# Kernel optimization log

Measured on AMD Instinct MI355X. Metric: run time of the kernel, lower is better.

The kernel has to match this reference:

```python
import jax, jax.numpy as jnp
import numpy as np

NUM_LAYERS = 2
FEATURES = 128
INPUT_SIZE = 128
HIDDEN = 512
BATCH = 128
SEQ_LEN = 512
PRED_LEN = 128


def _uniform(key, shape, fan):
    bound = 1.0 / np.sqrt(fan)
    return jax.random.uniform(key, shape, jnp.float32, -bound, bound)


def setup_inputs() -> dict:
    key = jax.random.key(0)
    ks = jax.random.split(key, 14)
    inp = {}
    inp["x"] = jax.random.normal(ks[0], (BATCH, SEQ_LEN, FEATURES), jnp.float32)
    # encoder Linear(features -> input_size)
    inp["enc_w"] = _uniform(ks[1], (INPUT_SIZE, FEATURES), FEATURES)
    inp["enc_b"] = _uniform(ks[2], (INPUT_SIZE,), FEATURES)
    # decoder Linear(hidden -> input_size)
    inp["dec_w"] = _uniform(ks[3], (INPUT_SIZE, HIDDEN), HIDDEN)
    inp["dec_b"] = _uniform(ks[4], (INPUT_SIZE,), HIDDEN)
    # LSTM layer 0 (input_size -> hidden), gate order i,f,g,o as in PyTorch
    inp["wih0"] = _uniform(ks[5], (4 * HIDDEN, INPUT_SIZE), HIDDEN)
    inp["whh0"] = _uniform(ks[6], (4 * HIDDEN, HIDDEN), HIDDEN)
    inp["bih0"] = _uniform(ks[7], (4 * HIDDEN,), HIDDEN)
    inp["bhh0"] = _uniform(ks[8], (4 * HIDDEN,), HIDDEN)
    # LSTM layer 1 (hidden -> hidden)
    inp["wih1"] = _uniform(ks[9], (4 * HIDDEN, HIDDEN), HIDDEN)
    inp["whh1"] = _uniform(ks[10], (4 * HIDDEN, HIDDEN), HIDDEN)
    inp["bih1"] = _uniform(ks[11], (4 * HIDDEN,), HIDDEN)
    inp["bhh1"] = _uniform(ks[12], (4 * HIDDEN,), HIDDEN)
    inp["pred_len"] = PRED_LEN
    return inp


def _lstm_cell(h, c, inp, wih, whh, bih, bhh):
    g = inp @ wih.T + bih + h @ whh.T + bhh  # [B, 4H]
    i, f, gg, o = jnp.split(g, 4, axis=-1)
    c = jax.nn.sigmoid(f) * c + jax.nn.sigmoid(i) * jnp.tanh(gg)
    h = jax.nn.sigmoid(o) * jnp.tanh(c)
    return h, c


def reference(x, enc_w, enc_b, dec_w, dec_b, wih0, whh0, bih0, bhh0,
              wih1, whh1, bih1, bhh1, pred_len):
    B, S, Fdim = x.shape
    T = S + pred_len - 1
    # pad x to T steps; beyond S the input comes from the previous output
    x_pad = jnp.concatenate([x, jnp.zeros((B, pred_len - 1, Fdim), x.dtype)], axis=1)
    x_t = jnp.transpose(x_pad, (1, 0, 2))  # [T, B, F]

    def step(carry, xs):
        h0, c0, h1, c1, prev_out = carry
        xt, t = xs
        inp = jnp.where(t < S, xt, prev_out)
        e = inp @ enc_w.T + enc_b                    # encoder
        h0, c0 = _lstm_cell(h0, c0, e, wih0, whh0, bih0, bhh0)
        h1, c1 = _lstm_cell(h1, c1, h0, wih1, whh1, bih1, bhh1)
        out = h1 @ dec_w.T + dec_b                   # decoder
        return (h0, c0, h1, c1, out), out

    z = jnp.zeros((B, HIDDEN), x.dtype)
    init = (z, z, z, z, jnp.zeros((B, Fdim), x.dtype))
    _, outs = jax.lax.scan(step, init, (x_t, jnp.arange(T)))
    # keep steps idx >= S-1 (pred_len outputs), back to [B, pred_len, input_size]
    return jnp.transpose(outs[S - 1:], (1, 0, 2))
```

## Files before the change

kernel.cpp:

```cpp
#include <hip/hip_runtime.h>
#include <math.h>

#define HID 512
#define FEAT 128
#define SEQL 512
#define PREDL 128
#define NWG 256
#define HK 516
#define EK 132

__device__ __forceinline__ float sigf_(float x) { return 1.0f / (1.0f + __expf(-x)); }
__device__ __forceinline__ float tanh_(float x) {
  float ax = fabsf(x);
  float e2 = __expf(-2.0f * ax);
  return copysignf((1.0f - e2) / (1.0f + e2), x);
}

__device__ __forceinline__ void stg_sc(float* p, float v) {
  __hip_atomic_store(p, v, __ATOMIC_RELAXED, __HIP_MEMORY_SCOPE_AGENT);
}

__device__ __forceinline__ void bar_arrive(int* __restrict__ bar, int grp,
                                           int phase, int tid, bool& last) {
  __syncthreads();
  if (tid == 0) {
    const int a = __hip_atomic_fetch_add(bar + grp * 32, 1, __ATOMIC_RELAXED,
                                         __HIP_MEMORY_SCOPE_AGENT);
    last = (a == 32 * phase - 1);
    if (last)
      __hip_atomic_store(bar + 512 + grp * 32, phase, __ATOMIC_RELAXED,
                         __HIP_MEMORY_SCOPE_AGENT);
  }
  asm volatile("" ::: "memory");
}
__device__ __forceinline__ void bar_wait(int* __restrict__ bar, int grp,
                                         int phase, int tid, bool last) {
  asm volatile("" ::: "memory");
  if (tid == 0 && !last) {
    while (__hip_atomic_load(bar + 512 + grp * 32, __ATOMIC_RELAXED,
                             __HIP_MEMORY_SCOPE_AGENT) < phase)
      __builtin_amdgcn_s_sleep(1);
  }
  __syncthreads();
}

__device__ __forceinline__ void stage_h(float* __restrict__ dst,
                                        const float* __restrict__ src,
                                        int b0, int tid) {
  const int kb = tid >> 2;
  const int bq = (tid & 3) * 4;
  const float* p0 = src + ((size_t)kb) * 128 + b0 + bq;
  const float* p1 = src + ((size_t)kb + 128) * 128 + b0 + bq;
  const float* p2 = src + ((size_t)kb + 256) * 128 + b0 + bq;
  const float* p3 = src + ((size_t)kb + 384) * 128 + b0 + bq;
  float4 r0, r1, r2, r3;
  asm volatile(
      "global_load_dwordx4 %0, %4, off sc0 sc1\n\t"
      "global_load_dwordx4 %1, %5, off sc0 sc1\n\t"
      "global_load_dwordx4 %2, %6, off sc0 sc1\n\t"
      "global_load_dwordx4 %3, %7, off sc0 sc1\n\t"
      "s_waitcnt vmcnt(0)"
      : "=&v"(r0), "=&v"(r1), "=&v"(r2), "=&v"(r3)
      : "v"(p0), "v"(p1), "v"(p2), "v"(p3)
      : "memory");
  dst[(bq + 0) * HK + kb] = r0.x;  dst[(bq + 1) * HK + kb] = r0.y;
  dst[(bq + 2) * HK + kb] = r0.z;  dst[(bq + 3) * HK + kb] = r0.w;
  dst[(bq + 0) * HK + kb + 128] = r1.x;  dst[(bq + 1) * HK + kb + 128] = r1.y;
  dst[(bq + 2) * HK + kb + 128] = r1.z;  dst[(bq + 3) * HK + kb + 128] = r1.w;
  dst[(bq + 0) * HK + kb + 256] = r2.x;  dst[(bq + 1) * HK + kb + 256] = r2.y;
  dst[(bq + 2) * HK + kb + 256] = r2.z;  dst[(bq + 3) * HK + kb + 256] = r2.w;
  dst[(bq + 0) * HK + kb + 384] = r3.x;  dst[(bq + 1) * HK + kb + 384] = r3.y;
  dst[(bq + 2) * HK + kb + 384] = r3.z;  dst[(bq + 3) * HK + kb + 384] = r3.w;
}

__device__ __forceinline__ void stage_x(float* __restrict__ dst,
                                        const float* __restrict__ x, int t,
                                        int b0, int tid) {
  const int bb = tid >> 5;
  const int fq = (tid & 31) * 4;
  const float4 v =
      *(const float4*)(x + ((size_t)(b0 + bb) * SEQL + t) * FEAT + fq);
  *(float4*)(dst + bb * EK + fq) = v;
}

__device__ __forceinline__ void gemv512(float& a0, float& a1, float& a2,
                                        float& a3, const float* __restrict__ s,
                                        const float4* __restrict__ w0,
                                        const float4* __restrict__ w1,
                                        const float4* __restrict__ w2,
                                        const float4* __restrict__ w3) {
#pragma unroll 2
  for (int k4 = 0; k4 < 128; ++k4) {
    const float4 sv = *(const float4*)(s + k4 * 4);
    float4 w;
    w = w0[k4]; a0 += w.x * sv.x + w.y * sv.y + w.z * sv.z + w.w * sv.w;
    w = w1[k4]; a1 += w.x * sv.x + w.y * sv.y + w.z * sv.z + w.w * sv.w;
    w = w2[k4]; a2 += w.x * sv.x + w.y * sv.y + w.z * sv.z + w.w * sv.w;
    w = w3[k4]; a3 += w.x * sv.x + w.y * sv.y + w.z * sv.z + w.w * sv.w;
  }
}
__device__ __forceinline__ void gemv128(float& a0, float& a1, float& a2,
                                        float& a3, const float* __restrict__ s,
                                        const float4* __restrict__ w0,
                                        const float4* __restrict__ w1,
                                        const float4* __restrict__ w2,
                                        const float4* __restrict__ w3) {
#pragma unroll 4
  for (int k4 = 0; k4 < 32; ++k4) {
    const float4 sv = *(const float4*)(s + k4 * 4);
    float4 w;
    w = w0[k4]; a0 += w.x * sv.x + w.y * sv.y + w.z * sv.z + w.w * sv.w;
    w = w1[k4]; a1 += w.x * sv.x + w.y * sv.y + w.z * sv.z + w.w * sv.w;
    w = w2[k4]; a2 += w.x * sv.x + w.y * sv.y + w.z * sv.z + w.w * sv.w;
    w = w3[k4]; a3 += w.x * sv.x + w.y * sv.y + w.z * sv.z + w.w * sv.w;
  }
}

__device__ __forceinline__ void act_store(float a0, float a1, float a2,
                                          float a3, float& c_reg,
                                          float* __restrict__ HoutT,
                                          size_t cit) {
  const float ig = sigf_(a0), fg = sigf_(a1);
  const float gg = tanh_(a2), og = sigf_(a3);
  const float cn = fg * c_reg + ig * gg;
  c_reg = cn;
  stg_sc(HoutT + cit, og * tanh_(cn));
}

__global__ __launch_bounds__(512, 2) void k_persist(
    const float* __restrict__ x,
    const float* __restrict__ enc_w, const float* __restrict__ enc_b,
    const float* __restrict__ wih0, const float* __restrict__ whh0,
    const float* __restrict__ bih0, const float* __restrict__ bhh0,
    const float* __restrict__ wih1, const float* __restrict__ whh1,
    const float* __restrict__ bih1, const float* __restrict__ bhh1,
    const float* __restrict__ dec_w, const float* __restrict__ dec_b,
    const float* __restrict__ Wcomp, const float* __restrict__ bcomp,
    float* __restrict__ h0A, float* __restrict__ h0B,
    float* __restrict__ h1A, float* __restrict__ h1B,
    int* __restrict__ bar, float* __restrict__ out) {
  __shared__ float s_h0[16 * HK];
  __shared__ float s_h1[16 * HK];
  __shared__ float s_x[16 * EK];
  __shared__ float s_e[16 * EK];

  const int wg = blockIdx.x;
  const int tid = threadIdx.x;
  const int ut = (wg & 7) * 4 + ((wg >> 3) & 3);
  const int bt = wg >> 5;
  const int b0 = bt * 16;
  const int half = tid >> 8;
  const int t8 = tid & 255;
  const int u = t8 >> 4, b = t8 & 15;
  const int ug = ut * 16 + u;
  const size_t cit = (size_t)ug * 128 + b0 + b;

  float* h0b[2] = {h0A, h0B};
  float* h1b[2] = {h1A, h1B};
  const float* sh0row = s_h0 + b * HK;
  const float* sh1row = s_h1 + b * HK;
  const float* serow  = s_e + b * EK;

  const float4* e0p = (const float4*)(wih0 + (size_t)ug * FEAT);
  const float4* e1p = (const float4*)(wih0 + (size_t)(512 + ug) * FEAT);
  const float4* e2p = (const float4*)(wih0 + (size_t)(1024 + ug) * FEAT);
  const float4* e3p = (const float4*)(wih0 + (size_t)(1536 + ug) * FEAT);
  const float4* H00 = (const float4*)(whh0 + (size_t)ug * HID);
  const float4* H01 = (const float4*)(whh0 + (size_t)(512 + ug) * HID);
  const float4* H02 = (const float4*)(whh0 + (size_t)(1024 + ug) * HID);
  const float4* H03 = (const float4*)(whh0 + (size_t)(1536 + ug) * HID);
  const float4* Wc0 = (const float4*)(Wcomp + (size_t)ug * HID);
  const float4* Wc1 = (const float4*)(Wcomp + (size_t)(512 + ug) * HID);
  const float4* Wc2 = (const float4*)(Wcomp + (size_t)(1024 + ug) * HID);
  const float4* Wc3 = (const float4*)(Wcomp + (size_t)(1536 + ug) * HID);
  const float4* I10 = (const float4*)(wih1 + (size_t)ug * HID);
  const float4* I11 = (const float4*)(wih1 + (size_t)(512 + ug) * HID);
  const float4* I12 = (const float4*)(wih1 + (size_t)(1024 + ug) * HID);
  const float4* I13 = (const float4*)(wih1 + (size_t)(1536 + ug) * HID);
  const float4* H10 = (const float4*)(whh1 + (size_t)ug * HID);
  const float4* H11 = (const float4*)(whh1 + (size_t)(512 + ug) * HID);
  const float4* H12 = (const float4*)(whh1 + (size_t)(1024 + ug) * HID);
  const float4* H13 = (const float4*)(whh1 + (size_t)(1536 + ug) * HID);
  const float bt00 = bih0[ug] + bhh0[ug];
  const float bt01 = bih0[512 + ug] + bhh0[512 + ug];
  const float bt02 = bih0[1024 + ug] + bhh0[1024 + ug];
  const float bt03 = bih0[1536 + ug] + bhh0[1536 + ug];
  const float ba00 = bt00 + bcomp[ug];
  const float ba01 = bt01 + bcomp[512 + ug];
  const float ba02 = bt02 + bcomp[1024 + ug];
  const float ba03 = bt03 + bcomp[1536 + ug];
  const float b10 = bih1[ug] + bhh1[ug];
  const float b11 = bih1[512 + ug] + bhh1[512 + ug];
  const float b12 = bih1[1024 + ug] + bhh1[1024 + ug];
  const float b13 = bih1[1536 + ug] + bhh1[1536 + ug];

  const int eb = tid & 15;
  const int f0 = (tid >> 4) * 4;
  const float4* ew0 = (const float4*)(enc_w + (size_t)f0 * FEAT);
  const float4* ew1 = (const float4*)(enc_w + (size_t)(f0 + 1) * FEAT);
  const float4* ew2 = (const float4*)(enc_w + (size_t)(f0 + 2) * FEAT);
  const float4* ew3 = (const float4*)(enc_w + (size_t)(f0 + 3) * FEAT);
  const float encb0 = enc_b[f0], encb1 = enc_b[f0 + 1];
  const float encb2 = enc_b[f0 + 2], encb3 = enc_b[f0 + 3];
  const float* sxrow = s_x + eb * EK;

  const int is_dec = (half == 1) && (((wg >> 3) & 3) == 0);
  const int jdec = (wg & 7) * 16 + (t8 >> 4);
  const int bd = t8 & 15;
  const float4* decr = (const float4*)(dec_w + (size_t)jdec * HID);
  const float decb = dec_b[jdec];

  float c_reg = 0.0f;
  int ph = 0;
  bool last = false;

  stage_x(s_x, x, 0, b0, tid);
  for (int t = 0; t < SEQL; ++t) {
    const float* h0in = h0b[(t + 1) & 1];
    float* h0out = h0b[t & 1];
    const float* h1in = h1b[t & 1];
    float* h1out = h1b[(t + 1) & 1];

    stage_h(s_h0, h0in, b0, tid);
    stage_h(s_h1, h1in, b0, tid);
    __syncthreads();

    {
      float a0 = encb0, a1 = encb1, a2 = encb2, a3 = encb3;
      gemv128(a0, a1, a2, a3, sxrow, ew0, ew1, ew2, ew3);
      *(float4*)(s_e + eb * EK + f0) = make_float4(a0, a1, a2, a3);
    }
    __syncthreads();

    if (half == 0) {
      float a0 = bt00, a1 = bt01, a2 = bt02, a3 = bt03;
      gemv512(a0, a1, a2, a3, sh0row, H00, H01, H02, H03);
      gemv128(a0, a1, a2, a3, serow, e0p, e1p, e2p, e3p);
      act_store(a0, a1, a2, a3, c_reg, h0out, cit);
    } else if (t > 0) {
      float a0 = b10, a1 = b11, a2 = b12, a3 = b13;
      gemv512(a0, a1, a2, a3, sh0row, I10, I11, I12, I13);
      gemv512(a0, a1, a2, a3, sh1row, H10, H11, H12, H13);
      act_store(a0, a1, a2, a3, c_reg, h1out, cit);
    }
    bar_arrive(bar, bt, ++ph, tid, last);
    if (t + 1 < SEQL) stage_x(s_x, x, t + 1, b0, tid);
    bar_wait(bar, bt, ph, tid, last);
  }

  stage_h(s_h0, h0b[1], b0, tid);
  stage_h(s_h1, h1b[0], b0, tid);
  __syncthreads();
  if (half == 1) {
    float a0 = b10, a1 = b11, a2 = b12, a3 = b13;
    gemv512(a0, a1, a2, a3, sh0row, I10, I11, I12, I13);
    gemv512(a0, a1, a2, a3, sh1row, H10, H11, H12, H13);
    act_store(a0, a1, a2, a3, c_reg, h1b[1], cit);
  }
  bar_arrive(bar, bt, ++ph, tid, last);
  bar_wait(bar, bt, ph, tid, last);

  for (int t = SEQL; t < SEQL + PREDL - 1; ++t) {
    const float* h1prev = h1b[(t + 1) & 1];
    const float* h0prev = h0b[(t + 1) & 1];
    float* h0cur = h0b[t & 1];
    float* h1cur = h1b[t & 1];

    stage_h(s_h1, h1prev, b0, tid);
    stage_h(s_h0, h0prev, b0, tid);
    __syncthreads();
    if (half == 0) {
      float a0 = ba00, a1 = ba01, a2 = ba02, a3 = ba03;
      gemv512(a0, a1, a2, a3, sh1row, Wc0, Wc1, Wc2, Wc3);
      gemv512(a0, a1, a2, a3, sh0row, H00, H01, H02, H03);
      act_store(a0, a1, a2, a3, c_reg, h0cur, cit);
    } else if (is_dec) {
      float acc = decb;
      const float* srow = s_h1 + bd * HK;
#pragma unroll 2
      for (int k4 = 0; k4 < 128; ++k4) {
        const float4 sv = *(const float4*)(srow + k4 * 4);
        const float4 w = decr[k4];
        acc += w.x * sv.x + w.y * sv.y + w.z * sv.z + w.w * sv.w;
      }
      out[((size_t)(b0 + bd) * PREDL + (t - SEQL)) * FEAT + jdec] = acc;
    }
    bar_arrive(bar, bt, ++ph, tid, last);
    bar_wait(bar, bt, ph, tid, last);

    stage_h(s_h0, h0cur, b0, tid);
    __syncthreads();
    if (half == 1) {
      float a0 = b10, a1 = b11, a2 = b12, a3 = b13;
      gemv512(a0, a1, a2, a3, sh0row, I10, I11, I12, I13);
      gemv512(a0, a1, a2, a3, sh1row, H10, H11, H12, H13);
      act_store(a0, a1, a2, a3, c_reg, h1cur, cit);
    }
    bar_arrive(bar, bt, ++ph, tid, last);
    bar_wait(bar, bt, ph, tid, last);
  }

  stage_h(s_h1, h1b[0], b0, tid);
  __syncthreads();
  if (is_dec) {
    float acc = decb;
    const float* srow = s_h1 + bd * HK;
#pragma unroll 2
    for (int k4 = 0; k4 < 128; ++k4) {
      const float4 sv = *(const float4*)(srow + k4 * 4);
      const float4 w = decr[k4];
      acc += w.x * sv.x + w.y * sv.y + w.z * sv.z + w.w * sv.w;
    }
    out[((size_t)(b0 + bd) * PREDL + (PREDL - 1)) * FEAT + jdec] = acc;
  }
}

__global__ void k_b1(const float* __restrict__ enc_w,
                     const float* __restrict__ dec_w, float* __restrict__ B1) {
  const int idx = blockIdx.x * 256 + threadIdx.x;
  const int j = idx >> 9, m = idx & 511;
  float acc = 0.0f;
  for (int k = 0; k < FEAT; ++k) acc += enc_w[j * FEAT + k] * dec_w[k * HID + m];
  B1[idx] = acc;
}
__global__ void k_wcomp(const float* __restrict__ wih0,
                        const float* __restrict__ B1, float* __restrict__ W) {
  const size_t idx = (size_t)blockIdx.x * 256 + threadIdx.x;
  const int n = (int)(idx >> 9), m = (int)(idx & 511);
  float acc = 0.0f;
  for (int k = 0; k < FEAT; ++k) acc += wih0[n * FEAT + k] * B1[k * HID + m];
  W[idx] = acc;
}
__global__ void k_te(const float* __restrict__ enc_w,
                     const float* __restrict__ enc_b,
                     const float* __restrict__ dec_b, float* __restrict__ te) {
  const int j = threadIdx.x;
  float acc = enc_b[j];
  for (int k = 0; k < FEAT; ++k) acc += dec_b[k] * enc_w[j * FEAT + k];
  te[j] = acc;
}
__global__ void k_bcomp(const float* __restrict__ wih0,
                        const float* __restrict__ te, float* __restrict__ bc) {
  const int n = blockIdx.x * 256 + threadIdx.x;
  float acc = 0.0f;
  for (int j = 0; j < FEAT; ++j) acc += wih0[n * FEAT + j] * te[j];
  bc[n] = acc;
}

extern "C" void kernel_launch(void* const* d_in, const int* in_sizes, int n_in,
                              void* d_out, int out_size, void* d_ws,
                              size_t ws_size, hipStream_t stream) {
  const float* x     = (const float*)d_in[0];
  const float* enc_w = (const float*)d_in[1];
  const float* enc_b = (const float*)d_in[2];
  const float* dec_w = (const float*)d_in[3];
  const float* dec_b = (const float*)d_in[4];
  const float* wih0  = (const float*)d_in[5];
  const float* whh0  = (const float*)d_in[6];
  const float* bih0  = (const float*)d_in[7];
  const float* bhh0  = (const float*)d_in[8];
  const float* wih1  = (const float*)d_in[9];
  const float* whh1  = (const float*)d_in[10];
  const float* bih1  = (const float*)d_in[11];
  const float* bhh1  = (const float*)d_in[12];
  float* out = (float*)d_out;

  float* ws = (float*)d_ws;
  float* h0A   = ws;
  float* h0B   = ws + 65536;
  float* h1A   = ws + 131072;
  float* h1B   = ws + 196608;
  int*   bar   = (int*)(ws + 262144);
  float* Wcomp = ws + 263168;
  float* B1    = ws + 1311744;
  float* te    = ws + 1377280;
  float* bcomp = ws + 1377408;

  hipMemsetAsync(ws, 0, (size_t)263168 * sizeof(float) + 4096, stream);

  k_b1<<<256, 256, 0, stream>>>(enc_w, dec_w, B1);
  k_wcomp<<<4096, 256, 0, stream>>>(wih0, B1, Wcomp);
  k_te<<<1, 128, 0, stream>>>(enc_w, enc_b, dec_b, te);
  k_bcomp<<<8, 256, 0, stream>>>(wih0, te, bcomp);

  k_persist<<<NWG, 512, 0, stream>>>(
      x, enc_w, enc_b, wih0, whh0, bih0, bhh0, wih1, whh1, bih1, bhh1,
      dec_w, dec_b, Wcomp, bcomp, h0A, h0B, h1A, h1B, bar, out);
}
```

Measured before the change: 38.40 ms.

## Interleave gate weights for packed FMA and split-K autoregressive steps across halves

Precomputes gate-interleaved weight layouts (Wa8, Wf8, wih04, enc4) so each thread reads all four gates for one k with a single float4 and accumulates with packed 2-wide FMAs. In the autoregressive phase both thread halves now split the K dimension of each cell and reduce through shared memory, and the decoder is spread across all threads with an 8-way split-K. Both h buffers are staged with one batched load sequence, and launch bounds drop to one block per CU. The goal is to cut the serial per-step GEMV latency and underused threads. The cost is extra prep kernels, more shared memory and syncs, and lower occupancy.

```diff
diff --git a/kernel.cpp b/kernel.cpp
--- a/kernel.cpp
+++ b/kernel.cpp
@@ -8,6 +8,8 @@
 #define NWG 256
 #define HK 516
 #define EK 132
+
+typedef float v2f __attribute__((ext_vector_type(2)));
 
 __device__ __forceinline__ float sigf_(float x) { return 1.0f / (1.0f + __expf(-x)); }
 __device__ __forceinline__ float tanh_(float x) {
@@ -44,12 +46,60 @@
   __syncthreads();
 }
 
-__device__ __forceinline__ void stage_h(float* __restrict__ dst,
-                                        const float* __restrict__ src,
-                                        int b0, int tid) {
+__device__ __forceinline__ void stage_h2(float* __restrict__ dA,
+                                         const float* __restrict__ sA,
+                                         float* __restrict__ dB,
+                                         const float* __restrict__ sB,
+                                         int b0, int tid) {
   const int kb = tid >> 2;
   const int bq = (tid & 3) * 4;
-  const float* p0 = src + ((size_t)kb) * 128 + b0 + bq;
+  const float* a0 = sA + (size_t)kb * 128 + b0 + bq;
+  const float* a1 = sA + ((size_t)kb + 128) * 128 + b0 + bq;
+  const float* a2 = sA + ((size_t)kb + 256) * 128 + b0 + bq;
+  const float* a3 = sA + ((size_t)kb + 384) * 128 + b0 + bq;
+  const float* c0 = sB + (size_t)kb * 128 + b0 + bq;
+  const float* c1 = sB + ((size_t)kb + 128) * 128 + b0 + bq;
+  const float* c2 = sB + ((size_t)kb + 256) * 128 + b0 + bq;
+  const float* c3 = sB + ((size_t)kb + 384) * 128 + b0 + bq;
+  float4 r0, r1, r2, r3, q0, q1, q2, q3;
+  asm volatile(
+      "global_load_dwordx4 %0, %8, off sc0 sc1\n\t"
+      "global_load_dwordx4 %1, %9, off sc0 sc1\n\t"
+      "global_load_dwordx4 %2, %10, off sc0 sc1\n\t"
+      "global_load_dwordx4 %3, %11, off sc0 sc1\n\t"
+      "global_load_dwordx4 %4, %12, off sc0 sc1\n\t"
+      "global_load_dwordx4 %5, %13, off sc0 sc1\n\t"
+      "global_load_dwordx4 %6, %14, off sc0 sc1\n\t"
+      "global_load_dwordx4 %7, %15, off sc0 sc1\n\t"
+      "s_waitcnt vmcnt(0)"
+      : "=&v"(r0), "=&v"(r1), "=&v"(r2), "=&v"(r3),
+        "=&v"(q0), "=&v"(q1), "=&v"(q2), "=&v"(q3)
+      : "v"(a0), "v"(a1), "v"(a2), "v"(a3),
+        "v"(c0), "v"(c1), "v"(c2), "v"(c3)
+      : "memory");
+  dA[(bq + 0) * HK + kb] = r0.x; dA[(bq + 1) * HK + kb] = r0.y;
+  dA[(bq + 2) * HK + kb] = r0.z; dA[(bq + 3) * HK + kb] = r0.w;
+  dA[(bq + 0) * HK + kb + 128] = r1.x; dA[(bq + 1) * HK + kb + 128] = r1.y;
+  dA[(bq + 2) * HK + kb + 128] = r1.z; dA[(bq + 3) * HK + kb + 128] = r1.w;
+  dA[(bq + 0) * HK + kb + 256] = r2.x; dA[(bq + 1) * HK + kb + 256] = r2.y;
+  dA[(bq + 2) * HK + kb + 256] = r2.z; dA[(bq + 3) * HK + kb + 256] = r2.w;
+  dA[(bq + 0) * HK + kb + 384] = r3.x; dA[(bq + 1) * HK + kb + 384] = r3.y;
+  dA[(bq + 2) * HK + kb + 384] = r3.z; dA[(bq + 3) * HK + kb + 384] = r3.w;
+  dB[(bq + 0) * HK + kb] = q0.x; dB[(bq + 1) * HK + kb] = q0.y;
+  dB[(bq + 2) * HK + kb] = q0.z; dB[(bq + 3) * HK + kb] = q0.w;
+  dB[(bq + 0) * HK + kb + 128] = q1.x; dB[(bq + 1) * HK + kb + 128] = q1.y;
+  dB[(bq + 2) * HK + kb + 128] = q1.z; dB[(bq + 3) * HK + kb + 128] = q1.w;
+  dB[(bq + 0) * HK + kb + 256] = q2.x; dB[(bq + 1) * HK + kb + 256] = q2.y;
+  dB[(bq + 2) * HK + kb + 256] = q2.z; dB[(bq + 3) * HK + kb + 256] = q2.w;
+  dB[(bq + 0) * HK + kb + 384] = q3.x; dB[(bq + 1) * HK + kb + 384] = q3.y;
+  dB[(bq + 2) * HK + kb + 384] = q3.z; dB[(bq + 3) * HK + kb + 384] = q3.w;
+}
+__device__ __forceinline__ void stage_h1t(float* __restrict__ dst,
+                                          const float* __restrict__ src,
+                                          int b0, int tid) {
+  const int kb = tid >> 2;
+  const int bq = (tid & 3) * 4;
+  const float* p0 = src + (size_t)kb * 128 + b0 + bq;
   const float* p1 = src + ((size_t)kb + 128) * 128 + b0 + bq;
   const float* p2 = src + ((size_t)kb + 256) * 128 + b0 + bq;
   const float* p3 = src + ((size_t)kb + 384) * 128 + b0 + bq;
@@ -63,16 +113,15 @@
       : "=&v"(r0), "=&v"(r1), "=&v"(r2), "=&v"(r3)
       : "v"(p0), "v"(p1), "v"(p2), "v"(p3)
       : "memory");
-  dst[(bq + 0) * HK + kb] = r0.x;  dst[(bq + 1) * HK + kb] = r0.y;
-  dst[(bq + 2) * HK + kb] = r0.z;  dst[(bq + 3) * HK + kb] = r0.w;
-  dst[(bq + 0) * HK + kb + 128] = r1.x;  dst[(bq + 1) * HK + kb + 128] = r1.y;
-  dst[(bq + 2) * HK + kb + 128] = r1.z;  dst[(bq + 3) * HK + kb + 128] = r1.w;
-  dst[(bq + 0) * HK + kb + 256] = r2.x;  dst[(bq + 1) * HK + kb + 256] = r2.y;
-  dst[(bq + 2) * HK + kb + 256] = r2.z;  dst[(bq + 3) * HK + kb + 256] = r2.w;
-  dst[(bq + 0) * HK + kb + 384] = r3.x;  dst[(bq + 1) * HK + kb + 384] = r3.y;
-  dst[(bq + 2) * HK + kb + 384] = r3.z;  dst[(bq + 3) * HK + kb + 384] = r3.w;
-}
-
+  dst[(bq + 0) * HK + kb] = r0.x; dst[(bq + 1) * HK + kb] = r0.y;
+  dst[(bq + 2) * HK + kb] = r0.z; dst[(bq + 3) * HK + kb] = r0.w;
+  dst[(bq + 0) * HK + kb + 128] = r1.x; dst[(bq + 1) * HK + kb + 128] = r1.y;
+  dst[(bq + 2) * HK + kb + 128] = r1.z; dst[(bq + 3) * HK + kb + 128] = r1.w;
+  dst[(bq + 0) * HK + kb + 256] = r2.x; dst[(bq + 1) * HK + kb + 256] = r2.y;
+  dst[(bq + 2) * HK + kb + 256] = r2.z; dst[(bq + 3) * HK + kb + 256] = r2.w;
+  dst[(bq + 0) * HK + kb + 384] = r3.x; dst[(bq + 1) * HK + kb + 384] = r3.y;
+  dst[(bq + 2) * HK + kb + 384] = r3.z; dst[(bq + 3) * HK + kb + 384] = r3.w;
+}
 __device__ __forceinline__ void stage_x(float* __restrict__ dst,
                                         const float* __restrict__ x, int t,
                                         int b0, int tid) {
@@ -83,59 +132,80 @@
   *(float4*)(dst + bb * EK + fq) = v;
 }
 
-__device__ __forceinline__ void gemv512(float& a0, float& a1, float& a2,
-                                        float& a3, const float* __restrict__ s,
-                                        const float4* __restrict__ w0,
-                                        const float4* __restrict__ w1,
-                                        const float4* __restrict__ w2,
-                                        const float4* __restrict__ w3) {
+__device__ __forceinline__ void pkf(v2f& a01, v2f& a23, float4 w, float h) {
+  v2f hh; hh[0] = h; hh[1] = h;
+  v2f lo; lo[0] = w.x; lo[1] = w.y;
+  v2f hi; hi[0] = w.z; hi[1] = w.w;
+  a01 = __builtin_elementwise_fma(lo, hh, a01);
+  a23 = __builtin_elementwise_fma(hi, hh, a23);
+}
+__device__ __forceinline__ void gemv_fused8(v2f& a01, v2f& a23,
+                                            const float4* __restrict__ W8,
+                                            size_t base,
+                                            const float* __restrict__ rA,
+                                            const float* __restrict__ rB,
+                                            int k4b, int k4e) {
 #pragma unroll 2
-  for (int k4 = 0; k4 < 128; ++k4) {
-    const float4 sv = *(const float4*)(s + k4 * 4);
-    float4 w;
-    w = w0[k4]; a0 += w.x * sv.x + w.y * sv.y + w.z * sv.z + w.w * sv.w;
-    w = w1[k4]; a1 += w.x * sv.x + w.y * sv.y + w.z * sv.z + w.w * sv.w;
-    w = w2[k4]; a2 += w.x * sv.x + w.y * sv.y + w.z * sv.z + w.w * sv.w;
-    w = w3[k4]; a3 += w.x * sv.x + w.y * sv.y + w.z * sv.z + w.w * sv.w;
-  }
-}
-__device__ __forceinline__ void gemv128(float& a0, float& a1, float& a2,
-                                        float& a3, const float* __restrict__ s,
-                                        const float4* __restrict__ w0,
-                                        const float4* __restrict__ w1,
-                                        const float4* __restrict__ w2,
-                                        const float4* __restrict__ w3) {
+  for (int k4 = k4b; k4 < k4e; ++k4) {
+    const float4 hA = *(const float4*)(rA + k4 * 4);
+    const float4 hB = *(const float4*)(rB + k4 * 4);
+    const size_t o = base + (size_t)k4 * 8;
+    pkf(a01, a23, W8[o + 0], hA.x); pkf(a01, a23, W8[o + 1], hB.x);
+    pkf(a01, a23, W8[o + 2], hA.y); pkf(a01, a23, W8[o + 3], hB.y);
+    pkf(a01, a23, W8[o + 4], hA.z); pkf(a01, a23, W8[o + 5], hB.z);
+    pkf(a01, a23, W8[o + 6], hA.w); pkf(a01, a23, W8[o + 7], hB.w);
+  }
+}
+__device__ __forceinline__ void gemv_half8(v2f& a01, v2f& a23,
+                                           const float4* __restrict__ W8,
+                                           size_t base, int sel,
+                                           const float* __restrict__ row,
+                                           int nk4) {
 #pragma unroll 4
-  for (int k4 = 0; k4 < 32; ++k4) {
-    const float4 sv = *(const float4*)(s + k4 * 4);
-    float4 w;
-    w = w0[k4]; a0 += w.x * sv.x + w.y * sv.y + w.z * sv.z + w.w * sv.w;
-    w = w1[k4]; a1 += w.x * sv.x + w.y * sv.y + w.z * sv.z + w.w * sv.w;
-    w = w2[k4]; a2 += w.x * sv.x + w.y * sv.y + w.z * sv.z + w.w * sv.w;
-    w = w3[k4]; a3 += w.x * sv.x + w.y * sv.y + w.z * sv.z + w.w * sv.w;
-  }
-}
-
-__device__ __forceinline__ void act_store(float a0, float a1, float a2,
-                                          float a3, float& c_reg,
+  for (int k4 = 0; k4 < nk4; ++k4) {
+    const float4 h = *(const float4*)(row + k4 * 4);
+    const size_t o = base + (size_t)k4 * 8 + sel;
+    pkf(a01, a23, W8[o + 0], h.x);
+    pkf(a01, a23, W8[o + 2], h.y);
+    pkf(a01, a23, W8[o + 4], h.z);
+    pkf(a01, a23, W8[o + 6], h.w);
+  }
+}
+__device__ __forceinline__ void gemv_p4(v2f& a01, v2f& a23,
+                                        const float4* __restrict__ W4,
+                                        size_t base,
+                                        const float* __restrict__ row,
+                                        int nk4) {
+#pragma unroll 4
+  for (int k4 = 0; k4 < nk4; ++k4) {
+    const float4 h = *(const float4*)(row + k4 * 4);
+    const size_t o = base + (size_t)k4 * 4;
+    pkf(a01, a23, W4[o + 0], h.x);
+    pkf(a01, a23, W4[o + 1], h.y);
+    pkf(a01, a23, W4[o + 2], h.z);
+    pkf(a01, a23, W4[o + 3], h.w);
+  }
+}
+
+__device__ __forceinline__ void act_store(v2f a01, v2f a23, float& c_reg,
                                           float* __restrict__ HoutT,
                                           size_t cit) {
-  const float ig = sigf_(a0), fg = sigf_(a1);
-  const float gg = tanh_(a2), og = sigf_(a3);
+  const float ig = sigf_(a01[0]), fg = sigf_(a01[1]);
+  const float gg = tanh_(a23[0]), og = sigf_(a23[1]);
   const float cn = fg * c_reg + ig * gg;
   c_reg = cn;
   stg_sc(HoutT + cit, og * tanh_(cn));
 }
 
-__global__ __launch_bounds__(512, 2) void k_persist(
+__global__ __launch_bounds__(512, 1) void k_persist(
     const float* __restrict__ x,
-    const float* __restrict__ enc_w, const float* __restrict__ enc_b,
-    const float* __restrict__ wih0, const float* __restrict__ whh0,
+    const float* __restrict__ enc4, const float* __restrict__ enc_b,
+    const float* __restrict__ wih04, const float* __restrict__ Wa8,
+    const float* __restrict__ Wf8,
     const float* __restrict__ bih0, const float* __restrict__ bhh0,
-    const float* __restrict__ wih1, const float* __restrict__ whh1,
     const float* __restrict__ bih1, const float* __restrict__ bhh1,
     const float* __restrict__ dec_w, const float* __restrict__ dec_b,
-    const float* __restrict__ Wcomp, const float* __restrict__ bcomp,
+    const float* __restrict__ bcomp,
     float* __restrict__ h0A, float* __restrict__ h0B,
     float* __restrict__ h1A, float* __restrict__ h1B,
     int* __restrict__ bar, float* __restrict__ out) {
@@ -143,13 +213,13 @@
   __shared__ float s_h1[16 * HK];
   __shared__ float s_x[16 * EK];
   __shared__ float s_e[16 * EK];
+  __shared__ float s_red[1536];
 
   const int wg = blockIdx.x;
   const int tid = threadIdx.x;
   const int ut = (wg & 7) * 4 + ((wg >> 3) & 3);
   const int bt = wg >> 5;
   const int b0 = bt * 16;
-  const int half = tid >> 8;
   const int t8 = tid & 255;
   const int u = t8 >> 4, b = t8 & 15;
   const int ug = ut * 16 + u;
@@ -159,28 +229,15 @@
   float* h1b[2] = {h1A, h1B};
   const float* sh0row = s_h0 + b * HK;
   const float* sh1row = s_h1 + b * HK;
-  const float* serow  = s_e + b * EK;
-
-  const float4* e0p = (const float4*)(wih0 + (size_t)ug * FEAT);
-  const float4* e1p = (const float4*)(wih0 + (size_t)(512 + ug) * FEAT);
-  const float4* e2p = (const float4*)(wih0 + (size_t)(1024 + ug) * FEAT);
-  const float4* e3p = (const float4*)(wih0 + (size_t)(1536 + ug) * FEAT);
-  const float4* H00 = (const float4*)(whh0 + (size_t)ug * HID);
-  const float4* H01 = (const float4*)(whh0 + (size_t)(512 + ug) * HID);
-  const float4* H02 = (const float4*)(whh0 + (size_t)(1024 + ug) * HID);
-  const float4* H03 = (const float4*)(whh0 + (size_t)(1536 + ug) * HID);
-  const float4* Wc0 = (const float4*)(Wcomp + (size_t)ug * HID);
-  const float4* Wc1 = (const float4*)(Wcomp + (size_t)(512 + ug) * HID);
-  const float4* Wc2 = (const float4*)(Wcomp + (size_t)(1024 + ug) * HID);
-  const float4* Wc3 = (const float4*)(Wcomp + (size_t)(1536 + ug) * HID);
-  const float4* I10 = (const float4*)(wih1 + (size_t)ug * HID);
-  const float4* I11 = (const float4*)(wih1 + (size_t)(512 + ug) * HID);
-  const float4* I12 = (const float4*)(wih1 + (size_t)(1024 + ug) * HID);
-  const float4* I13 = (const float4*)(wih1 + (size_t)(1536 + ug) * HID);
-  const float4* H10 = (const float4*)(whh1 + (size_t)ug * HID);
-  const float4* H11 = (const float4*)(whh1 + (size_t)(512 + ug) * HID);
-  const float4* H12 = (const float4*)(whh1 + (size_t)(1024 + ug) * HID);
-  const float4* H13 = (const float4*)(whh1 + (size_t)(1536 + ug) * HID);
+  const float* serow = s_e + b * EK;
+
+  const float4* W8a = (const float4*)Wa8;
+  const float4* W8f = (const float4*)Wf8;
+  const float4* W4i = (const float4*)wih04;
+  const float4* W4e = (const float4*)enc4;
+  const size_t baseG = (size_t)ug * 1024;
+  const size_t baseI = (size_t)ug * 128;
+
   const float bt00 = bih0[ug] + bhh0[ug];
   const float bt01 = bih0[512 + ug] + bhh0[512 + ug];
   const float bt02 = bih0[1024 + ug] + bhh0[1024 + ug];
@@ -195,20 +252,16 @@
   const float b13 = bih1[1536 + ug] + bhh1[1536 + ug];
 
   const int eb = tid & 15;
-  const int f0 = (tid >> 4) * 4;
-  const float4* ew0 = (const float4*)(enc_w + (size_t)f0 * FEAT);
-  const float4* ew1 = (const float4*)(enc_w + (size_t)(f0 + 1) * FEAT);
-  const float4* ew2 = (const float4*)(enc_w + (size_t)(f0 + 2) * FEAT);
-  const float4* ew3 = (const float4*)(enc_w + (size_t)(f0 + 3) * FEAT);
-  const float encb0 = enc_b[f0], encb1 = enc_b[f0 + 1];
-  const float encb2 = enc_b[f0 + 2], encb3 = enc_b[f0 + 3];
+  const int fb = tid >> 4;
+  const size_t baseE = (size_t)fb * 128;
+  const float eb0 = enc_b[fb * 4], eb1 = enc_b[fb * 4 + 1];
+  const float eb2 = enc_b[fb * 4 + 2], eb3 = enc_b[fb * 4 + 3];
   const float* sxrow = s_x + eb * EK;
 
-  const int is_dec = (half == 1) && (((wg >> 3) & 3) == 0);
-  const int jdec = (wg & 7) * 16 + (t8 >> 4);
-  const int bd = t8 & 15;
-  const float4* decr = (const float4*)(dec_w + (size_t)jdec * HID);
-  const float decb = dec_b[jdec];
+  const int djj = tid >> 7, dbb = (tid >> 3) & 15, dk8 = tid & 7;
+  const int jd = (wg & 31) * 4 + djj;
+  const float4* decr = (const float4*)(dec_w + (size_t)jd * HID);
+  const float* dhrow = s_h1 + dbb * HK;
 
   float c_reg = 0.0f;
   int ph = 0;
@@ -221,41 +274,53 @@
     const float* h1in = h1b[t & 1];
     float* h1out = h1b[(t + 1) & 1];
 
-    stage_h(s_h0, h0in, b0, tid);
-    stage_h(s_h1, h1in, b0, tid);
+    stage_h2(s_h0, h0in, s_h1, h1in, b0, tid);
     __syncthreads();
 
     {
-      float a0 = encb0, a1 = encb1, a2 = encb2, a3 = encb3;
-      gemv128(a0, a1, a2, a3, sxrow, ew0, ew1, ew2, ew3);
-      *(float4*)(s_e + eb * EK + f0) = make_float4(a0, a1, a2, a3);
+      v2f a01; a01[0] = eb0; a01[1] = eb1;
+      v2f a23; a23[0] = eb2; a23[1] = eb3;
+      gemv_p4(a01, a23, W4e, baseE, sxrow, 32);
+      *(float4*)(s_e + eb * EK + fb * 4) =
+          make_float4(a01[0], a01[1], a23[0], a23[1]);
     }
     __syncthreads();
 
-    if (half == 0) {
-      float a0 = bt00, a1 = bt01, a2 = bt02, a3 = bt03;
-      gemv512(a0, a1, a2, a3, sh0row, H00, H01, H02, H03);
-      gemv128(a0, a1, a2, a3, serow, e0p, e1p, e2p, e3p);
-      act_store(a0, a1, a2, a3, c_reg, h0out, cit);
+    if (tid < 256) {
+      v2f a01; a01[0] = bt00; a01[1] = bt01;
+      v2f a23; a23[0] = bt02; a23[1] = bt03;
+      gemv_half8(a01, a23, W8a, baseG, 1, sh0row, 128);
+      gemv_p4(a01, a23, W4i, baseI, serow, 32);
+      act_store(a01, a23, c_reg, h0out, cit);
     } else if (t > 0) {
-      float a0 = b10, a1 = b11, a2 = b12, a3 = b13;
-      gemv512(a0, a1, a2, a3, sh0row, I10, I11, I12, I13);
-      gemv512(a0, a1, a2, a3, sh1row, H10, H11, H12, H13);
-      act_store(a0, a1, a2, a3, c_reg, h1out, cit);
+      v2f a01; a01[0] = b10; a01[1] = b11;
+      v2f a23; a23[0] = b12; a23[1] = b13;
+      gemv_fused8(a01, a23, W8f, baseG, sh0row, sh1row, 0, 128);
+      act_store(a01, a23, c_reg, h1out, cit);
     }
     bar_arrive(bar, bt, ++ph, tid, last);
     if (t + 1 < SEQL) stage_x(s_x, x, t + 1, b0, tid);
     bar_wait(bar, bt, ph, tid, last);
   }
 
-  stage_h(s_h0, h0b[1], b0, tid);
-  stage_h(s_h1, h1b[0], b0, tid);
+  stage_h2(s_h0, h0b[1], s_h1, h1b[0], b0, tid);
   __syncthreads();
-  if (half == 1) {
-    float a0 = b10, a1 = b11, a2 = b12, a3 = b13;
-    gemv512(a0, a1, a2, a3, sh0row, I10, I11, I12, I13);
-    gemv512(a0, a1, a2, a3, sh1row, H10, H11, H12, H13);
-    act_store(a0, a1, a2, a3, c_reg, h1b[1], cit);
+  {
+    const int own = (tid >= 256);
+    v2f a01, a23;
+    if (own) { a01[0] = b10; a01[1] = b11; a23[0] = b12; a23[1] = b13; }
+    else { a01[0] = 0; a01[1] = 0; a23[0] = 0; a23[1] = 0; }
+    const int kb4 = own ? 0 : 64;
+    gemv_fused8(a01, a23, W8f, baseG, sh0row, sh1row, kb4, kb4 + 64);
+    if (!own) {
+      *(float4*)(s_red + t8 * 4) = make_float4(a01[0], a01[1], a23[0], a23[1]);
+    }
+    __syncthreads();
+    if (own) {
+      const float4 p = *(const float4*)(s_red + t8 * 4);
+      a01[0] += p.x; a01[1] += p.y; a23[0] += p.z; a23[1] += p.w;
+      act_store(a01, a23, c_reg, h1b[1], cit);
+    }
   }
   bar_arrive(bar, bt, ++ph, tid, last);
   bar_wait(bar, bt, ph, tid, last);
@@ -266,52 +331,81 @@
     float* h0cur = h0b[t & 1];
     float* h1cur = h1b[t & 1];
 
-    stage_h(s_h1, h1prev, b0, tid);
-    stage_h(s_h0, h0prev, b0, tid);
+    stage_h2(s_h1, h1prev, s_h0, h0prev, b0, tid);
     __syncthreads();
-    if (half == 0) {
-      float a0 = ba00, a1 = ba01, a2 = ba02, a3 = ba03;
-      gemv512(a0, a1, a2, a3, sh1row, Wc0, Wc1, Wc2, Wc3);
-      gemv512(a0, a1, a2, a3, sh0row, H00, H01, H02, H03);
-      act_store(a0, a1, a2, a3, c_reg, h0cur, cit);
-    } else if (is_dec) {
-      float acc = decb;
-      const float* srow = s_h1 + bd * HK;
-#pragma unroll 2
-      for (int k4 = 0; k4 < 128; ++k4) {
-        const float4 sv = *(const float4*)(srow + k4 * 4);
+    {
+      const int own = (tid < 256);
+      v2f a01, a23;
+      if (own) { a01[0] = ba00; a01[1] = ba01; a23[0] = ba02; a23[1] = ba03; }
+      else { a01[0] = 0; a01[1] = 0; a23[0] = 0; a23[1] = 0; }
+      const int kb4 = own ? 0 : 64;
+      gemv_fused8(a01, a23, W8a, baseG, sh1row, sh0row, kb4, kb4 + 64);
+      float dacc = 0.0f;
+#pragma unroll 4
+      for (int k4 = dk8 * 16; k4 < dk8 * 16 + 16; ++k4) {
         const float4 w = decr[k4];
-        acc += w.x * sv.x + w.y * sv.y + w.z * sv.z + w.w * sv.w;
+        const float4 h = *(const float4*)(dhrow + k4 * 4);
+        dacc += w.x * h.x + w.y * h.y + w.z * h.z + w.w * h.w;
       }
-      out[((size_t)(b0 + bd) * PREDL + (t - SEQL)) * FEAT + jdec] = acc;
+      s_red[1024 + tid] = dacc;
+      if (!own)
+        *(float4*)(s_red + t8 * 4) = make_float4(a01[0], a01[1], a23[0], a23[1]);
+      __syncthreads();
+      if (own) {
+        const float4 p = *(const float4*)(s_red + t8 * 4);
+        a01[0] += p.x; a01[1] += p.y; a23[0] += p.z; a23[1] += p.w;
+        act_store(a01, a23, c_reg, h0cur, cit);
+      }
+      if (dk8 == 0) {
+        float s = dec_b[jd];
+#pragma unroll
+        for (int i = 0; i < 8; ++i) s += s_red[1024 + tid + i];
+        out[((size_t)(b0 + dbb) * PREDL + (t - SEQL)) * FEAT + jd] = s;
+      }
     }
     bar_arrive(bar, bt, ++ph, tid, last);
     bar_wait(bar, bt, ph, tid, last);
 
-    stage_h(s_h0, h0cur, b0, tid);
+    stage_h1t(s_h0, h0cur, b0, tid);
     __syncthreads();
-    if (half == 1) {
-      float a0 = b10, a1 = b11, a2 = b12, a3 = b13;
-      gemv512(a0, a1, a2, a3, sh0row, I10, I11, I12, I13);
-      gemv512(a0, a1, a2, a3, sh1row, H10, H11, H12, H13);
-      act_store(a0, a1, a2, a3, c_reg, h1cur, cit);
+    {
+      const int own = (tid >= 256);
+      v2f a01, a23;
+      if (own) { a01[0] = b10; a01[1] = b11; a23[0] = b12; a23[1] = b13; }
+      else { a01[0] = 0; a01[1] = 0; a23[0] = 0; a23[1] = 0; }
+      const int kb4 = own ? 0 : 64;
+      gemv_fused8(a01, a23, W8f, baseG, sh0row, sh1row, kb4, kb4 + 64);
+      if (!own)
+        *(float4*)(s_red + t8 * 4) = make_float4(a01[0], a01[1], a23[0], a23[1]);
+      __syncthreads();
+      if (own) {
+        const float4 p = *(const float4*)(s_red + t8 * 4);
+        a01[0] += p.x; a01[1] += p.y; a23[0] += p.z; a23[1] += p.w;
+        act_store(a01, a23, c_reg, h1cur, cit);
+      }
     }
     bar_arrive(bar, bt, ++ph, tid, last);
     bar_wait(bar, bt, ph, tid, last);
   }
 
-  stage_h(s_h1, h1b[0], b0, tid);
+  stage_h1t(s_h1, h1b[0], b0, tid);
   __syncthreads();
-  if (is_dec) {
-    float acc = decb;
-    const float* srow = s_h1 + bd * HK;
-#pragma unroll 2
-    for (int k4 = 0; k4 < 128; ++k4) {
-      const float4 sv = *(const float4*)(srow + k4 * 4);
+  {
+    float dacc = 0.0f;
+#pragma unroll 4
+    for (int k4 = dk8 * 16; k4 < dk8 * 16 + 16; ++k4) {
       const float4 w = decr[k4];
-      acc += w.x * sv.x + w.y * sv.y + w.z * sv.z + w.w * sv.w;
-    }
-    out[((size_t)(b0 + bd) * PREDL + (PREDL - 1)) * FEAT + jdec] = acc;
+      const float4 h = *(const float4*)(dhrow + k4 * 4);
+      dacc += w.x * h.x + w.y * h.y + w.z * h.z + w.w * h.w;
+    }
+    s_red[1024 + tid] = dacc;
+    __syncthreads();
+    if (dk8 == 0) {
+      float s = dec_b[jd];
+#pragma unroll
+      for (int i = 0; i < 8; ++i) s += s_red[1024 + tid + i];
+      out[((size_t)(b0 + dbb) * PREDL + (PREDL - 1)) * FEAT + jd] = s;
+    }
   }
 }
 
@@ -323,14 +417,6 @@
   for (int k = 0; k < FEAT; ++k) acc += enc_w[j * FEAT + k] * dec_w[k * HID + m];
   B1[idx] = acc;
 }
-__global__ void k_wcomp(const float* __restrict__ wih0,
-                        const float* __restrict__ B1, float* __restrict__ W) {
-  const size_t idx = (size_t)blockIdx.x * 256 + threadIdx.x;
-  const int n = (int)(idx >> 9), m = (int)(idx & 511);
-  float acc = 0.0f;
-  for (int k = 0; k < FEAT; ++k) acc += wih0[n * FEAT + k] * B1[k * HID + m];
-  W[idx] = acc;
-}
 __global__ void k_te(const float* __restrict__ enc_w,
                      const float* __restrict__ enc_b,
                      const float* __restrict__ dec_b, float* __restrict__ te) {
@@ -346,6 +432,71 @@
   for (int j = 0; j < FEAT; ++j) acc += wih0[n * FEAT + j] * te[j];
   bc[n] = acc;
 }
+__global__ void k_wa8(const float* __restrict__ wih0,
+                      const float* __restrict__ B1,
+                      const float* __restrict__ whh0, float* __restrict__ W) {
+  const int idx = blockIdx.x * 256 + threadIdx.x;
+  const int uu = idx >> 9, k = idx & 511;
+  float c[4];
+#pragma unroll
+  for (int g = 0; g < 4; ++g) {
+    const float* wr = wih0 + ((size_t)(g * 512 + uu)) * FEAT;
+    float acc = 0.0f;
+    for (int j = 0; j < FEAT; ++j) acc += wr[j] * B1[j * HID + k];
+    c[g] = acc;
+  }
+  float4* o = (float4*)(W + ((size_t)(uu * 512 + k)) * 8);
+  o[0] = make_float4(c[0], c[1], c[2], c[3]);
+  o[1] = make_float4(whh0[((size_t)uu) * 512 + k],
+                     whh0[((size_t)(512 + uu)) * 512 + k],
+                     whh0[((size_t)(1024 + uu)) * 512 + k],
+                     whh0[((size_t)(1536 + uu)) * 512 + k]);
+}
+__global__ void k_wf8(const float* __restrict__ wih1,
+                      const float* __restrict__ whh1, float* __restrict__ W) {
+  const int idx = blockIdx.x * 256 + threadIdx.x;
+  const int uu = idx >> 9, k = idx & 511;
+  float4* o = (float4*)(W + ((size_t)(uu * 512 + k)) * 8);
+  o[0] = make_float4(wih1[((size_t)uu) * 512 + k],
+                     wih1[((size_t)(512 + uu)) * 512 + k],
+                     wih1[((size_t)(1024 + uu)) * 512 + k],
+                     wih1[((size_t)(1536 + uu)) * 512 + k]);
+  o[1] = make_float4(whh1[((size_t)uu) * 512 + k],
+                     whh1[((size_t)(512 + uu)) * 512 + k],
+                     whh1[((size_t)(1024 + uu)) * 512 + k],
+                     whh1[((size_t)(1536 + uu)) * 512 + k]);
+}
+__global__ void k_wih04(const float* __restrict__ wih0, float* __restrict__ W) {
+  const int idx = blockIdx.x * 256 + threadIdx.x;
+  const int uu = idx >> 7, k = idx & 127;
+  float4* o = (float4*)(W + ((size_t)idx) * 4);
+  o[0] = make_float4(wih0[((size_t)uu) * FEAT + k],
+                     wih0[((size_t)(512 + uu)) * FEAT + k],
+                     wih0[((size_t)(1024 + uu)) * FEAT + k],
+                     wih0[((size_t)(1536 + uu)) * FEAT + k]);
+}
+__global__ void k_enc4(const float* __restrict__ enc_w, float* __restrict__ W) {
+  const int idx = blockIdx.x * 256 + threadIdx.x;
+  const int fb = idx >> 7, k = idx & 127;
+  float4* o = (float4*)(W + ((size_t)idx) * 4);
+  o[0] = make_float4(enc_w[((size_t)(fb * 4 + 0)) * FEAT + k],
+                     enc_w[((size_t)(fb * 4 + 1)) * FEAT + k],
+                     enc_w[((size_t)(fb * 4 + 2)) * FEAT + k],
+                     enc_w[((size_t)(fb * 4 + 3)) * FEAT + k]);
+}
+
+#define WS_H0A 0
+#define WS_H0B 65536
+#define WS_H1A 131072
+#define WS_H1B 196608
+#define WS_BAR 262144
+#define WS_B1 263168
+#define WS_TE 328704
+#define WS_BCOMP 328832
+#define WS_WIH04 330880
+#define WS_ENC4 593024
+#define WS_WA8 609408
+#define WS_WF8 2706560
 
 extern "C" void kernel_launch(void* const* d_in, const int* in_sizes, int n_in,
                               void* d_out, int out_size, void* d_ws,
@@ -366,24 +517,30 @@
   float* out = (float*)d_out;
 
   float* ws = (float*)d_ws;
-  float* h0A   = ws;
-  float* h0B   = ws + 65536;
-  float* h1A   = ws + 131072;
-  float* h1B   = ws + 196608;
-  int*   bar   = (int*)(ws + 262144);
-  float* Wcomp = ws + 263168;
-  float* B1    = ws + 1311744;
-  float* te    = ws + 1377280;
-  float* bcomp = ws + 1377408;
-
-  hipMemsetAsync(ws, 0, (size_t)263168 * sizeof(float) + 4096, stream);
+  float* h0A = ws + WS_H0A;
+  float* h0B = ws + WS_H0B;
+  float* h1A = ws + WS_H1A;
+  float* h1B = ws + WS_H1B;
+  int* bar = (int*)(ws + WS_BAR);
+  float* B1 = ws + WS_B1;
+  float* te = ws + WS_TE;
+  float* bcomp = ws + WS_BCOMP;
+  float* wih04 = ws + WS_WIH04;
+  float* enc4 = ws + WS_ENC4;
+  float* Wa8 = ws + WS_WA8;
+  float* Wf8 = ws + WS_WF8;
+
+  hipMemsetAsync(ws, 0, (size_t)WS_B1 * sizeof(float), stream);
 
   k_b1<<<256, 256, 0, stream>>>(enc_w, dec_w, B1);
-  k_wcomp<<<4096, 256, 0, stream>>>(wih0, B1, Wcomp);
   k_te<<<1, 128, 0, stream>>>(enc_w, enc_b, dec_b, te);
   k_bcomp<<<8, 256, 0, stream>>>(wih0, te, bcomp);
+  k_wa8<<<1024, 256, 0, stream>>>(wih0, B1, whh0, Wa8);
+  k_wf8<<<1024, 256, 0, stream>>>(wih1, whh1, Wf8);
+  k_wih04<<<256, 256, 0, stream>>>(wih0, wih04);
+  k_enc4<<<16, 256, 0, stream>>>(enc_w, enc4);
 
   k_persist<<<NWG, 512, 0, stream>>>(
-      x, enc_w, enc_b, wih0, whh0, bih0, bhh0, wih1, whh1, bih1, bhh1,
-      dec_w, dec_b, Wcomp, bcomp, h0A, h0B, h1A, h1B, bar, out);
-}
+      x, enc4, enc_b, wih04, Wa8, Wf8, bih0, bhh0, bih1, bhh1,
+      dec_w, dec_b, bcomp, h0A, h0B, h1A, h1B, bar, out);
+}
```

New measurement: 37.38 ms. -2.7%, faster.
